# Kernel tuning notes

Hardware: AMD Instinct MI355X
Metric: run time of the kernel (lower is better)

## Reference

```python
import jax, jax.numpy as jnp
import numpy as np

NMS_MAX_OUTPUTS = 2000
CLS_SCORE_THRESH = 0.7
IOU_THRESH = 0.3
USE_SIDE_REFINE = False
B, N_ANCHORS, N_VALID, NUM_CLASSES = 4, 20000, 12000, 2


def setup_inputs() -> dict:
    key = jax.random.key(0)
    k = jax.random.split(key, 7)
    deltas = 0.5 * jax.random.normal(k[0], (B, N_ANCHORS, 2), jnp.float32)
    side_deltas = 0.5 * jax.random.normal(k[1], (B, N_ANCHORS, 1), jnp.float32)
    class_logits = 2.0 * jax.random.normal(k[2], (B, N_ANCHORS, NUM_CLASSES), jnp.float32)
    # CTPN-style anchors: fixed width 16, heights in [11, 280], on a ~1600px page
    cx = jax.random.uniform(k[3], (N_VALID,), jnp.float32, 8.0, 1592.0)
    cy = jax.random.uniform(k[4], (N_VALID,), jnp.float32, 0.0, 1600.0)
    h = jax.random.uniform(k[5], (N_VALID,), jnp.float32, 11.0, 280.0)
    valid_anchors = jnp.stack([cx - 8.0, cy - h * 0.5, cx + 8.0, cy + h * 0.5], axis=1)
    valid_indices = jnp.sort(
        jax.random.choice(k[6], N_ANCHORS, (N_VALID,), replace=False)
    ).astype(jnp.int32)
    return {
        "deltas": deltas,
        "side_deltas": side_deltas,
        "class_logits": class_logits,
        "valid_anchors": valid_anchors,
        "valid_indices": valid_indices,
    }


def apply_regress(deltas, side_deltas, anchors, use_side_refine):
    # deltas [B,V,2], side_deltas [B,V,1], anchors [V,4] -> [B,V,4]
    w = anchors[:, 2] - anchors[:, 0]
    h = anchors[:, 3] - anchors[:, 1]
    cx = (anchors[:, 0] + anchors[:, 2]) * 0.5
    cy = (anchors[:, 1] + anchors[:, 3]) * 0.5
    d = jnp.concatenate([deltas, side_deltas], axis=-1) * jnp.array([0.1, 0.2, 0.1], deltas.dtype)
    dy, dh, dx = d[..., 0], d[..., 1], d[..., 2]
    cy = cy + dy * h
    cx = cx + dx * w
    h = h * jnp.exp(dh)
    y1 = cy - h * 0.5
    y2 = cy + h * 0.5
    if use_side_refine:
        x1 = jnp.maximum(cx - w * 0.5, 0.0)
        x2 = cx + w * 0.5
    else:
        x1 = jnp.broadcast_to(anchors[:, 0], y1.shape)
        x2 = jnp.broadcast_to(anchors[:, 2], y1.shape)
    return jnp.stack([x1, y1, x2, y2], axis=-1)


def nms_single(boxes, scores, logits, max_out, iou_t, score_t):
    """Greedy NMS (tf.image.non_max_suppression semantics) + gather + pad_to_fixed_size."""
    V = boxes.shape[0]
    order = jnp.argsort(-jax.lax.stop_gradient(scores))
    b, s, l = boxes[order], scores[order], logits[order]
    bc = jax.lax.stop_gradient(b)  # suppression decisions are non-differentiable
    x1, y1, x2, y2 = bc[:, 0], bc[:, 1], bc[:, 2], bc[:, 3]
    areas = (x2 - x1) * (y2 - y1)
    idxs = jnp.arange(V)
    valid = jax.lax.stop_gradient(s) > score_t

    def body(i, keep):
        xx1 = jnp.maximum(x1[i], x1)
        yy1 = jnp.maximum(y1[i], y1)
        xx2 = jnp.minimum(x2[i], x2)
        yy2 = jnp.minimum(y2[i], y2)
        inter = jnp.maximum(xx2 - xx1, 0.0) * jnp.maximum(yy2 - yy1, 0.0)
        iou = inter / (areas[i] + areas - inter + 1e-10)
        sup = (iou > iou_t) & (idxs > i)
        return jnp.where(keep[i], keep & ~sup, keep)

    keep = jax.lax.fori_loop(0, V, body, valid)
    rank = jnp.cumsum(keep.astype(jnp.int32)) - 1
    sel = keep & (rank < max_out)
    dest = jnp.where(sel, rank, max_out)  # overflow rows parked at row max_out, sliced off
    tag = jnp.ones((V, 1), b.dtype)

    def pad_fixed(x):
        # append tag column of 1s for real rows, scatter to fixed size, zero-pad rest
        aug = jnp.where(sel[:, None], jnp.concatenate([x, tag], axis=1), 0.0)
        out = jnp.zeros((max_out + 1, aug.shape[1]), aug.dtype).at[dest].set(aug)
        return out[:max_out]

    return pad_fixed(b), pad_fixed(s[:, None]), pad_fixed(l)


def reference(deltas, side_deltas, class_logits, valid_anchors, valid_indices):
    d = jnp.take(deltas, valid_indices, axis=1)
    sd = jnp.take(side_deltas, valid_indices, axis=1)
    cl = jnp.take(class_logits, valid_indices, axis=1)
    class_scores = jax.nn.softmax(cl, axis=-1)
    fg_scores = jnp.max(class_scores[..., 1:], axis=-1)  # [B,V]
    proposals = apply_regress(d, sd, valid_anchors, USE_SIDE_REFINE)  # [B,V,4]
    f = lambda bb, ss, ll: nms_single(bb, ss, ll, NMS_MAX_OUTPUTS, IOU_THRESH, CLS_SCORE_THRESH)
    boxes, box_scores, out_logits = jax.vmap(f)(proposals, fg_scores, cl)
    return boxes, box_scores, out_logits
```

## Files before the change

### kernel.cpp

```cpp
#include <hip/hip_runtime.h>
#include <cstdint>
#include <cstddef>

typedef unsigned long long u64;
typedef unsigned int u32;
typedef u32 u32x4 __attribute__((ext_vector_type(4)));

#define AS1 __attribute__((address_space(1)))
#define AS3 __attribute__((address_space(3)))

constexpr int kB = 4;
constexpr int kNA = 20000;
constexpr int kV = 12000;
constexpr int kCAP = 5120;
constexpr int kW = kCAP / 64;
constexpr int kIC = 256;
constexpr int kNCH = kCAP / kIC;
constexpr int kMAXOUT = 2000;
constexpr int kGPB = 20;
constexpr int kSWG = kB * kGPB;
constexpr int kMWG = kB * kW * kNCH / 4;
constexpr float kIOU = 0.3f;
constexpr float kSCORE = 0.7f;

static __device__ __forceinline__ u64 greedy64(u64 freeS, u32 d_lo, u32 d_hi) {
  u64 keptS;
  asm volatile(
      "s_mov_b64 s[40:41], %[free]\n\t"
      "s_mov_b64 s[42:43], 0\n\t"
      "GRD_%=:\n\t"
      "s_ff1_i32_b64 s44, s[40:41]\n\t"
      "s_cmp_eq_i32 s44, -1\n\t"
      "s_cbranch_scc1 GRDEND_%=\n\t"
      "s_bitset1_b64 s[42:43], s44\n\t"
      "s_bitset0_b64 s[40:41], s44\n\t"
      "v_readlane_b32 s46, %[dlo], s44\n\t"
      "v_readlane_b32 s47, %[dhi], s44\n\t"
      "s_nop 4\n\t"
      "s_andn2_b64 s[40:41], s[40:41], s[46:47]\n\t"
      "s_branch GRD_%=\n\t"
      "GRDEND_%=:\n\t"
      "s_mov_b64 %[kept], s[42:43]\n\t"
      : [kept] "=&s"(keptS)
      : [free] "s"(freeS), [dlo] "v"(d_lo), [dhi] "v"(d_hi)
      : "s40", "s41", "s42", "s43", "s44", "s45", "s46", "s47", "scc");
  return keptS;
}

__device__ __forceinline__ u64 waveOr64(u64 v) {
  v |= __shfl_xor((unsigned long long)v, 32, 64);
  v |= __shfl_xor((unsigned long long)v, 16, 64);
  v |= __shfl_xor((unsigned long long)v, 8, 64);
  v |= __shfl_xor((unsigned long long)v, 4, 64);
  v |= __shfl_xor((unsigned long long)v, 2, 64);
  v |= __shfl_xor((unsigned long long)v, 1, 64);
  return v;
}

__device__ __forceinline__ u64 readlane64u(u64 v, int l) {
  u32 lo = __builtin_amdgcn_readlane((u32)v, (u32)l);
  u32 hi = __builtin_amdgcn_readlane((u32)(v >> 32), (u32)l);
  return ((u64)hi << 32) | lo;
}

__global__ __launch_bounds__(256) void stage_score(
    const float* __restrict__ deltas, const float* __restrict__ logits,
    const float* __restrict__ anchors, const int* __restrict__ vidx,
    u32* __restrict__ counts, u64* __restrict__ keys,
    float* __restrict__ rec_y1, float* __restrict__ rec_y2,
    float* __restrict__ rec_l0, float* __restrict__ rec_l1) {
  int t = blockIdx.x * 256 + threadIdx.x;
  if (t >= kB * kV) return;
  int b = t / kV, i = t - b * kV;
  int lane = threadIdx.x & 63;
  int idx = vidx[i];
  float2 lg = *(const float2*)(logits + ((size_t)b * kNA + idx) * 2);
  float score = 1.0f / (1.0f + expf(lg.x - lg.y));
  if (!(score > kSCORE)) return;
  float2 dd = *(const float2*)(deltas + ((size_t)b * kNA + idx) * 2);
  float4 a = *(const float4*)(anchors + (size_t)i * 4);
  float h = a.w - a.y;
  float cy = (a.y + a.w) * 0.5f + (dd.x * 0.1f) * h;
  float hn = h * expf(dd.y * 0.2f);
  rec_y1[t] = cy - hn * 0.5f;
  rec_y2[t] = cy + hn * 0.5f;
  rec_l0[t] = lg.x;
  rec_l1[t] = lg.y;
  u64 act = __ballot(1);
  int b0 = (int)__builtin_amdgcn_readfirstlane((u32)b);
  u64 sameb = __ballot(b == b0);
  u64 grp = (b == b0) ? sameb : (act & ~sameb);
  u32 cnt = (u32)__popcll(grp);
  int lead = (int)__ffsll((unsigned long long)grp) - 1;
  u32 base = 0;
  if (lane == lead) base = atomicAdd(&counts[b], cnt);
  base = (u32)__shfl((int)base, lead, 64);
  u32 pos = base + (u32)__popcll(grp & ((1ULL << lane) - 1ULL));
  if (pos < kCAP) {
    u64 key = ((u64)(0xFFFFFFFFu - __float_as_uint(score)) << 32) | (u32)i;
    keys[(size_t)b * kCAP + pos] = key;
  }
}

__global__ __launch_bounds__(256) void rank_sort_emit(
    const u32* __restrict__ counts, const u64* __restrict__ keys,
    const float* __restrict__ rec_y1, const float* __restrict__ rec_y2,
    const float* __restrict__ rec_l0, const float* __restrict__ rec_l1,
    const float* __restrict__ anchors,
    float4* __restrict__ sbox, float* __restrict__ sarea,
    float* __restrict__ ssc, float* __restrict__ sl0, float* __restrict__ sl1) {
  __shared__ u64 sk[kCAP];
  int b = blockIdx.x / (kCAP / 256);
  int chunk = blockIdx.x % (kCAP / 256);
  int tid = threadIdx.x;
  int cnt = (int)min(counts[b], (u32)kCAP);
  for (int e = tid; e < kCAP; e += 256)
    sk[e] = (e < cnt) ? keys[(size_t)b * kCAP + e] : ~0ULL;
  __syncthreads();
  int s = chunk * 256 + tid;
  if (s >= cnt) return;
  u64 ks = sk[s];
  int rank = 0;
  for (int j = 0; j < kCAP; j += 8) {
#pragma unroll
    for (int u = 0; u < 8; ++u) rank += (sk[j + u] < ks) ? 1 : 0;
  }
  int i = (int)(u32)ks;
  float sc = __uint_as_float(0xFFFFFFFFu - (u32)(ks >> 32));
  float x1 = anchors[(size_t)i * 4 + 0], x2 = anchors[(size_t)i * 4 + 2];
  float y1 = rec_y1[b * kV + i], y2 = rec_y2[b * kV + i];
  size_t o = (size_t)b * kCAP + rank;
  sbox[o] = make_float4(x1, y1, x2, y2);
  sarea[o] = (x2 - x1) * (y2 - y1);
  ssc[o] = sc;
  sl0[o] = rec_l0[b * kV + i];
  sl1[o] = rec_l1[b * kV + i];
}

__global__ __launch_bounds__(256) void fused_mask_scan(
    const u32* __restrict__ counts,
    const float4* __restrict__ sbox, const float* __restrict__ sarea,
    u64* __restrict__ mask, u32* __restrict__ colcnt, u64* __restrict__ pub,
    const float* __restrict__ ssc, const float* __restrict__ sl0,
    const float* __restrict__ sl1, float* __restrict__ out) {
  __shared__ __align__(16) char smem[20480];
  const int bid = blockIdx.x;

  if (bid >= kSWG) {
    float4* sbc = (float4*)smem;
    float* sac = (float*)(smem + 16384);
    int lane = threadIdx.x & 63;
    int wv = threadIdx.x >> 6;
    int gw = (bid - kSWG) * 4 + wv;
    int jb = gw / (kB * kNCH);
    int rest = gw - jb * (kB * kNCH);
    int bt = rest & 3;
    int ic = rest >> 2;
    int M = (int)min(counts[bt], (u32)kCAP);
    int W = (M + 63) >> 6;
    if (jb < W) {
      int ibeg = ic * kIC;
      int iend = min(min(M, jb * 64 + 64), ibeg + kIC);
      if (ibeg < iend) {
        const float4* pb = sbox + (size_t)bt * kCAP;
        const float* pa = sarea + (size_t)bt * kCAP;
        u64* mb = mask + (size_t)bt * ((size_t)kW * kCAP);
#pragma unroll
        for (int r = 0; r < kIC / 64; ++r) {
          int e = r * 64 + lane;
          sbc[wv * kIC + e] = pb[ibeg + e];
          sac[wv * kIC + e] = pa[ibeg + e];
        }
        int j = jb * 64 + lane;
        bool jv = (j < M);
        float4 bj = make_float4(0.f, 0.f, 0.f, 0.f);
        float aj = 0.f;
        if (jv) { bj = pb[j]; aj = pa[j]; }
        for (int b0 = ibeg; b0 < iend; b0 += 64) {
          int lim = min(iend - b0, 64);
          u64 mywm = 0;
#pragma unroll 4
          for (int k = 0; k < lim; ++k) {
            int e = b0 - ibeg + k;
            float4 bi = sbc[wv * kIC + e];
            float ai = sac[wv * kIC + e];
            float xx1 = fmaxf(bi.x, bj.x);
            float yy1 = fmaxf(bi.y, bj.y);
            float xx2 = fminf(bi.z, bj.z);
            float yy2 = fminf(bi.w, bj.w);
            float inter = fmaxf(xx2 - xx1, 0.0f) * fmaxf(yy2 - yy1, 0.0f);
            float iou = inter / (ai + aj - inter + 1e-10f);
            bool sup = jv && (j > b0 + k) && (iou > kIOU);
            u64 wm = __ballot(sup);
            if (k == lane) mywm = wm;
          }
          if (lane < lim)
            mb[(((size_t)(b0 >> 6)) * kW + jb) * 64 + lane] = mywm;
        }
      }
    }
    if (lane == 0)
      (void)__hip_atomic_fetch_add(&colcnt[bt * kW + jb], 1u, __ATOMIC_RELEASE,
                                   __HIP_MEMORY_SCOPE_AGENT);
    return;
  }

  if (threadIdx.x >= 64) return;
  u64* ownl = (u64*)smem;
  const int bt = bid & 3;
  const int g = bid >> 2;
  const int lane = threadIdx.x;
  const int M = (int)min(counts[bt], (u32)kCAP);
  const int W = (M + 63) >> 6;
  const int blk0 = 4 * g;
  if (blk0 >= W) return;
  const u64* mb = mask + (size_t)bt * ((size_t)kW * kCAP);
  u64* pp = pub + (size_t)(bt * kGPB) * 8;

#pragma unroll
  for (int c = 0; c < 4; ++c) {
    const u32* cp = &colcnt[bt * kW + 4 * g + c];
    while (__hip_atomic_load(cp, __ATOMIC_ACQUIRE, __HIP_MEMORY_SCOPE_AGENT) <
           (u32)kNCH)
      __builtin_amdgcn_s_sleep(16);
  }

#pragma unroll
  for (int J = 0; J < 4; ++J)
#pragma unroll
    for (int c = 0; c < 2; ++c)
      __builtin_amdgcn_global_load_lds(
          (const AS1 u32*)(mb + ((size_t)(blk0 + J) * kW + 4 * g + 2 * c) * 64 +
                           (size_t)lane * 2),
          (AS3 u32*)&ownl[(J * 2 + c) * 128], 16, 0, 0);

  u64 acc0 = 0, acc1 = 0, acc2 = 0, acc3 = 0;
  u32 cum = 0;
  const u64* qa = pp + (size_t)lane * 2;
  const u64* qb = pp + 128 + (size_t)(lane & 15) * 2;
  u64 pv[4][4];
  auto issuePf = [&](int w) {
#pragma unroll
    for (int c = 0; c < 4; ++c)
#pragma unroll
      for (int q = 0; q < 4; ++q)
        pv[c][q] = mb[((size_t)(4 * w + c) * kW + 4 * g + q) * 64 + lane];
  };
  int next = 0;
  if (g > 0) issuePf(0);
  while (next < g) {
    u32x4 ra, rb;
    asm volatile(
        "global_load_dwordx4 %0, %2, off sc0 sc1\n\t"
        "global_load_dwordx4 %1, %3, off sc0 sc1\n\t"
        "s_waitcnt vmcnt(0)"
        : "=&v"(ra), "=&v"(rb)
        : "v"(qa), "v"(qb)
        : "memory");
    u64 wA0 = ((u64)ra[1] << 32) | ra[0];
    u64 wA1 = ((u64)ra[3] << 32) | ra[2];
    u64 wB0 = ((u64)rb[1] << 32) | rb[0];
    u64 wB1 = ((u64)rb[3] << 32) | rb[2];
    u64 okA = __ballot(((wA0 & wA1) >> 63) != 0);
    u64 okB = __ballot(((wB0 & wB1) >> 63) != 0);
    bool adv = false;
    while (next < g) {
      const int w = next;
      u64 km0, km1, km2, km3;
      if (w < 16) {
        if (((okA >> (4 * w)) & 0xFULL) != 0xFULL) break;
        int L = 4 * w;
        km0 = (u64)(u32)readlane64u(wA0, L)     | ((u64)(u32)readlane64u(wA1, L) << 32);
        km1 = (u64)(u32)readlane64u(wA0, L + 1) | ((u64)(u32)readlane64u(wA1, L + 1) << 32);
        km2 = (u64)(u32)readlane64u(wA0, L + 2) | ((u64)(u32)readlane64u(wA1, L + 2) << 32);
        km3 = (u64)(u32)readlane64u(wA0, L + 3) | ((u64)(u32)readlane64u(wA1, L + 3) << 32);
      } else {
        int L = 4 * (w - 16);
        if (((okB >> L) & 0xFULL) != 0xFULL) break;
        km0 = (u64)(u32)readlane64u(wB0, L)     | ((u64)(u32)readlane64u(wB1, L) << 32);
        km1 = (u64)(u32)readlane64u(wB0, L + 1) | ((u64)(u32)readlane64u(wB1, L + 1) << 32);
        km2 = (u64)(u32)readlane64u(wB0, L + 2) | ((u64)(u32)readlane64u(wB1, L + 2) << 32);
        km3 = (u64)(u32)readlane64u(wB0, L + 3) | ((u64)(u32)readlane64u(wB1, L + 3) << 32);
      }
      cum += (u32)__popcll(km0) + (u32)__popcll(km1) +
             (u32)__popcll(km2) + (u32)__popcll(km3);
      if (km0 | km1 | km2 | km3) {
        u64 m0 = -(u64)((km0 >> lane) & 1ULL);
        u64 m1 = -(u64)((km1 >> lane) & 1ULL);
        u64 m2 = -(u64)((km2 >> lane) & 1ULL);
        u64 m3 = -(u64)((km3 >> lane) & 1ULL);
        acc0 |= waveOr64((pv[0][0] & m0) | (pv[1][0] & m1) | (pv[2][0] & m2) | (pv[3][0] & m3));
        acc1 |= waveOr64((pv[0][1] & m0) | (pv[1][1] & m1) | (pv[2][1] & m2) | (pv[3][1] & m3));
        acc2 |= waveOr64((pv[0][2] & m0) | (pv[1][2] & m1) | (pv[2][2] & m2) | (pv[3][2] & m3));
        acc3 |= waveOr64((pv[0][3] & m0) | (pv[1][3] & m1) | (pv[2][3] & m2) | (pv[3][3] & m3));
      }
      ++next;
      if (next < g) issuePf(next);
      adv = true;
    }
    if (next < g && !adv) __builtin_amdgcn_s_sleep(8);
  }
  __builtin_amdgcn_s_waitcnt(0x0070);

  u64 km[4];
  u32 cums[4];
  auto ownw = [&](int J, int q) -> u64 {
    return ownl[(J * 2 + (q >> 1)) * 128 + (q & 1) * 64 + lane];
  };
#define OWN_BLOCK(J, ACC)                                                     \
  {                                                                           \
    const int blk = blk0 + (J);                                               \
    cums[J] = cum;                                                            \
    u64 k = 0;                                                                \
    if (blk < W && (int)cum < kMAXOUT) {                                      \
      int remn = M - blk * 64;                                                \
      u64 validm = (remn >= 64) ? ~0ULL : ((1ULL << remn) - 1ULL);            \
      u64 freeb = ~(ACC)&validm;                                              \
      u32 flo = __builtin_amdgcn_readfirstlane((u32)freeb);                   \
      u32 fhi = __builtin_amdgcn_readfirstlane((u32)(freeb >> 32));           \
      u64 diag = ownw(J, J);                                                  \
      k = greedy64(((u64)fhi << 32) | flo, (u32)diag, (u32)(diag >> 32));     \
    }                                                                         \
    km[J] = k;                                                                \
    cum += (u32)__popcll(k);                                                  \
  }
  OWN_BLOCK(0, acc0)
  if (km[0]) {
    u64 m = -(u64)((km[0] >> lane) & 1ULL);
    acc1 |= waveOr64(ownw(0, 1) & m);
    acc2 |= waveOr64(ownw(0, 2) & m);
    acc3 |= waveOr64(ownw(0, 3) & m);
  }
  OWN_BLOCK(1, acc1)
  if (km[1]) {
    u64 m = -(u64)((km[1] >> lane) & 1ULL);
    acc2 |= waveOr64(ownw(1, 2) & m);
    acc3 |= waveOr64(ownw(1, 3) & m);
  }
  OWN_BLOCK(2, acc2)
  if (km[2]) {
    u64 m = -(u64)((km[2] >> lane) & 1ULL);
    acc3 |= waveOr64(ownw(2, 3) & m);
  }
  OWN_BLOCK(3, acc3)
#undef OWN_BLOCK

  if (lane == 0) {
    const u64 F = 1ULL << 63;
#pragma unroll
    for (int c = 0; c < 4; ++c) {
      (void)__hip_atomic_fetch_or(&pp[(size_t)g * 8 + 2 * c], F | (u64)(u32)km[c],
                                  __ATOMIC_RELAXED, __HIP_MEMORY_SCOPE_AGENT);
      (void)__hip_atomic_fetch_or(&pp[(size_t)g * 8 + 2 * c + 1],
                                  F | (u64)(u32)(km[c] >> 32),
                                  __ATOMIC_RELAXED, __HIP_MEMORY_SCOPE_AGENT);
    }
  }

  float* boxes = out;
  float* bscores = out + (size_t)kB * kMAXOUT * 5;
  float* blogits = out + (size_t)kB * kMAXOUT * 7;
  auto emit = [&](int i, int rank) {
    size_t o = (size_t)bt * kCAP + i;
    float4 bx = sbox[o];
    size_t t = (size_t)bt * kMAXOUT + rank;
    boxes[t * 5 + 0] = bx.x;
    boxes[t * 5 + 1] = bx.y;
    boxes[t * 5 + 2] = bx.z;
    boxes[t * 5 + 3] = bx.w;
    boxes[t * 5 + 4] = 1.0f;
    bscores[t * 2 + 0] = ssc[o];
    bscores[t * 2 + 1] = 1.0f;
    blogits[t * 3 + 0] = sl0[o];
    blogits[t * 3 + 1] = sl1[o];
    blogits[t * 3 + 2] = 1.0f;
  };
#pragma unroll
  for (int c = 0; c < 4; ++c) {
    if ((km[c] >> lane) & 1ULL) {
      int rank = (int)cums[c] + (int)__popcll(km[c] & ((1ULL << lane) - 1ULL));
      if (rank < kMAXOUT) emit((blk0 + c) * 64 + lane, rank);
    }
  }
}

extern "C" void kernel_launch(void* const* d_in, const int* in_sizes, int n_in,
                              void* d_out, int out_size, void* d_ws, size_t ws_size,
                              hipStream_t stream) {
  const float* deltas = (const float*)d_in[0];
  const float* logits = (const float*)d_in[2];
  const float* anchors = (const float*)d_in[3];
  const int* vidx = (const int*)d_in[4];
  float* out = (float*)d_out;

  char* p = (char*)d_ws;
  auto take = [&](size_t bytes) -> char* {
    char* r = p;
    p += (bytes + 255) & ~(size_t)255;
    return r;
  };
  u32* counts = (u32*)take(kB * sizeof(u32));
  u64* pub = (u64*)take((size_t)kB * kGPB * 8 * sizeof(u64));
  u32* colcnt = (u32*)take((size_t)kB * kW * sizeof(u32));
  u64* keys = (u64*)take((size_t)kB * kCAP * sizeof(u64));
  float* rec_y1 = (float*)take((size_t)kB * kV * sizeof(float));
  float* rec_y2 = (float*)take((size_t)kB * kV * sizeof(float));
  float* rec_l0 = (float*)take((size_t)kB * kV * sizeof(float));
  float* rec_l1 = (float*)take((size_t)kB * kV * sizeof(float));
  float4* sbox = (float4*)take((size_t)kB * kCAP * sizeof(float4));
  float* sarea = (float*)take((size_t)kB * kCAP * sizeof(float));
  float* ssc = (float*)take((size_t)kB * kCAP * sizeof(float));
  float* sl0 = (float*)take((size_t)kB * kCAP * sizeof(float));
  float* sl1 = (float*)take((size_t)kB * kCAP * sizeof(float));
  u64* mask = (u64*)take((size_t)kB * kCAP * kW * sizeof(u64) + 4096);

  (void)hipMemsetAsync(out, 0, (size_t)out_size * sizeof(float), stream);
  (void)hipMemsetAsync(counts, 0, 6656, stream);

  stage_score<<<(kB * kV + 255) / 256, 256, 0, stream>>>(
      deltas, logits, anchors, vidx, counts, keys, rec_y1, rec_y2, rec_l0, rec_l1);
  rank_sort_emit<<<kB * (kCAP / 256), 256, 0, stream>>>(
      counts, keys, rec_y1, rec_y2, rec_l0, rec_l1, anchors,
      sbox, sarea, ssc, sl0, sl1);
  fused_mask_scan<<<kSWG + kMWG, 256, 0, stream>>>(
      counts, sbox, sarea, mask, colcnt, pub, ssc, sl0, sl1, out);
}
```

Before: 346.5 us.

## Stage whole per-batch box set in LDS and loop mask workers over columns

Mask-building workgroups now load all 5120 sorted boxes and areas for one batch into 100KB of shared memory once. Each wave then loops over every column block, choosing its row chunk with a modular permutation, instead of each wave handling one (column, chunk) tile with a private 256-box LDS copy. The aim is to cut redundant global loads and the workgroup count, since 80 persistent groups replace the old many small ones. The trade-off is large LDS per block, which limits occupancy. Each group also walks columns in a fixed order, so scan blocks may wait longer before the column counters they poll are published.

```diff
diff --git a/kernel.cpp b/kernel.cpp
--- a/kernel.cpp
+++ b/kernel.cpp
@@ -19,7 +19,7 @@
 constexpr int kMAXOUT = 2000;
 constexpr int kGPB = 20;
 constexpr int kSWG = kB * kGPB;
-constexpr int kMWG = kB * kW * kNCH / 4;
+constexpr int kMWG = 80;
 constexpr float kIOU = 0.3f;
 constexpr float kSCORE = 0.7f;
 
@@ -143,47 +143,46 @@
     u64* __restrict__ mask, u32* __restrict__ colcnt, u64* __restrict__ pub,
     const float* __restrict__ ssc, const float* __restrict__ sl0,
     const float* __restrict__ sl1, float* __restrict__ out) {
-  __shared__ __align__(16) char smem[20480];
+  __shared__ __align__(16) char smem[102400];
   const int bid = blockIdx.x;
 
   if (bid >= kSWG) {
     float4* sbc = (float4*)smem;
-    float* sac = (float*)(smem + 16384);
-    int lane = threadIdx.x & 63;
-    int wv = threadIdx.x >> 6;
-    int gw = (bid - kSWG) * 4 + wv;
-    int jb = gw / (kB * kNCH);
-    int rest = gw - jb * (kB * kNCH);
-    int bt = rest & 3;
-    int ic = rest >> 2;
-    int M = (int)min(counts[bt], (u32)kCAP);
-    int W = (M + 63) >> 6;
-    if (jb < W) {
+    float* sac = (float*)(smem + 81920);
+    const int tid = threadIdx.x;
+    const int lane = tid & 63;
+    const int wv = tid >> 6;
+    const int w = bid - kSWG;
+    const int bt = w & 3;
+    const int r = (w >> 2) * 4 + wv;
+    const int M = (int)min(counts[bt], (u32)kCAP);
+    const int W = (M + 63) >> 6;
+    const float4* pb = sbox + (size_t)bt * kCAP;
+    const float* pa = sarea + (size_t)bt * kCAP;
+    u64* mb = mask + (size_t)bt * ((size_t)kW * kCAP);
+    for (int e = tid; e < kCAP; e += 256) {
+      sbc[e] = pb[e];
+      sac[e] = pa[e];
+    }
+    __syncthreads();
+    for (int jb = 0; jb < kW; ++jb) {
+      int ic = ((r - jb + 80) * 33) % 80;
+      if (ic >= kNCH) continue;
       int ibeg = ic * kIC;
       int iend = min(min(M, jb * 64 + 64), ibeg + kIC);
-      if (ibeg < iend) {
-        const float4* pb = sbox + (size_t)bt * kCAP;
-        const float* pa = sarea + (size_t)bt * kCAP;
-        u64* mb = mask + (size_t)bt * ((size_t)kW * kCAP);
-#pragma unroll
-        for (int r = 0; r < kIC / 64; ++r) {
-          int e = r * 64 + lane;
-          sbc[wv * kIC + e] = pb[ibeg + e];
-          sac[wv * kIC + e] = pa[ibeg + e];
-        }
+      if (jb < W && ibeg < iend) {
         int j = jb * 64 + lane;
         bool jv = (j < M);
         float4 bj = make_float4(0.f, 0.f, 0.f, 0.f);
         float aj = 0.f;
-        if (jv) { bj = pb[j]; aj = pa[j]; }
+        if (jv) { bj = sbc[j]; aj = sac[j]; }
         for (int b0 = ibeg; b0 < iend; b0 += 64) {
           int lim = min(iend - b0, 64);
           u64 mywm = 0;
 #pragma unroll 4
           for (int k = 0; k < lim; ++k) {
-            int e = b0 - ibeg + k;
-            float4 bi = sbc[wv * kIC + e];
-            float ai = sac[wv * kIC + e];
+            float4 bi = sbc[b0 + k];
+            float ai = sac[b0 + k];
             float xx1 = fmaxf(bi.x, bj.x);
             float yy1 = fmaxf(bi.y, bj.y);
             float xx2 = fminf(bi.z, bj.z);
@@ -198,10 +197,10 @@
             mb[(((size_t)(b0 >> 6)) * kW + jb) * 64 + lane] = mywm;
         }
       }
+      if (lane == 0)
+        (void)__hip_atomic_fetch_add(&colcnt[bt * kW + jb], 1u, __ATOMIC_RELEASE,
+                                     __HIP_MEMORY_SCOPE_AGENT);
     }
-    if (lane == 0)
-      (void)__hip_atomic_fetch_add(&colcnt[bt * kW + jb], 1u, __ATOMIC_RELEASE,
-                                   __HIP_MEMORY_SCOPE_AGENT);
     return;
   }
 
@@ -239,12 +238,12 @@
   const u64* qa = pp + (size_t)lane * 2;
   const u64* qb = pp + 128 + (size_t)(lane & 15) * 2;
   u64 pv[4][4];
-  auto issuePf = [&](int w) {
+  auto issuePf = [&](int w2) {
 #pragma unroll
     for (int c = 0; c < 4; ++c)
 #pragma unroll
       for (int q = 0; q < 4; ++q)
-        pv[c][q] = mb[((size_t)(4 * w + c) * kW + 4 * g + q) * 64 + lane];
+        pv[c][q] = mb[((size_t)(4 * w2 + c) * kW + 4 * g + q) * 64 + lane];
   };
   int next = 0;
   if (g > 0) issuePf(0);
@@ -265,17 +264,17 @@
     u64 okB = __ballot(((wB0 & wB1) >> 63) != 0);
     bool adv = false;
     while (next < g) {
-      const int w = next;
+      const int w2 = next;
       u64 km0, km1, km2, km3;
-      if (w < 16) {
-        if (((okA >> (4 * w)) & 0xFULL) != 0xFULL) break;
-        int L = 4 * w;
+      if (w2 < 16) {
+        if (((okA >> (4 * w2)) & 0xFULL) != 0xFULL) break;
+        int L = 4 * w2;
         km0 = (u64)(u32)readlane64u(wA0, L)     | ((u64)(u32)readlane64u(wA1, L) << 32);
         km1 = (u64)(u32)readlane64u(wA0, L + 1) | ((u64)(u32)readlane64u(wA1, L + 1) << 32);
         km2 = (u64)(u32)readlane64u(wA0, L + 2) | ((u64)(u32)readlane64u(wA1, L + 2) << 32);
         km3 = (u64)(u32)readlane64u(wA0, L + 3) | ((u64)(u32)readlane64u(wA1, L + 3) << 32);
       } else {
-        int L = 4 * (w - 16);
+        int L = 4 * (w2 - 16);
         if (((okB >> L) & 0xFULL) != 0xFULL) break;
         km0 = (u64)(u32)readlane64u(wB0, L)     | ((u64)(u32)readlane64u(wB1, L) << 32);
         km1 = (u64)(u32)readlane64u(wB0, L + 1) | ((u64)(u32)readlane64u(wB1, L + 1) << 32);
```

After: 513.3 us. 1.48x slower.
